# Kernel tuning notes

Measured on AMD Instinct MI355X. Metric: run time of the kernel, lower is better.

Reference implementation:

```python
import jax, jax.numpy as jnp
import numpy as np

N_NODES = 50000
N_EDGES = 625000
IN_DIM = 512
HID = 128
OUT_DIM = 40
N_LAYERS = 3


def setup_inputs() -> dict:
    key = jax.random.key(0)
    ks = jax.random.split(key, 12)
    features = jax.random.normal(ks[0], (N_NODES, IN_DIM), dtype=jnp.float32)
    src = jax.random.randint(ks[1], (N_EDGES,), 0, N_NODES, dtype=jnp.int32)
    dst = jax.random.randint(ks[2], (N_EDGES,), 0, N_NODES, dtype=jnp.int32)
    edge_w = jax.random.uniform(ks[3], (N_EDGES,), dtype=jnp.float32)
    s_in = 1.0 / np.sqrt(IN_DIM)
    s_h = 1.0 / np.sqrt(HID)
    emb_W = jax.random.uniform(ks[4], (IN_DIM, HID), jnp.float32, -s_in, s_in)
    emb_b = jax.random.uniform(ks[5], (HID,), jnp.float32, -s_in, s_in)
    W1 = jax.random.uniform(ks[6], (N_LAYERS, HID, HID), jnp.float32, -s_h, s_h)
    b1 = jax.random.uniform(ks[7], (N_LAYERS, HID), jnp.float32, -s_h, s_h)
    W2 = jax.random.uniform(ks[8], (N_LAYERS, HID, HID), jnp.float32, -s_h, s_h)
    b2 = jax.random.uniform(ks[9], (N_LAYERS, HID), jnp.float32, -s_h, s_h)
    ro_W = jax.random.uniform(ks[10], (HID, OUT_DIM), jnp.float32, -s_h, s_h)
    ro_b = jax.random.uniform(ks[11], (OUT_DIM,), jnp.float32, -s_h, s_h)
    return {"features": features, "src": src, "dst": dst, "edge_w": edge_w,
            "emb_W": emb_W, "emb_b": emb_b, "W1": W1, "b1": b1,
            "W2": W2, "b2": b2, "ro_W": ro_W, "ro_b": ro_b}


def reference(features, src, dst, edge_w, emb_W, emb_b, W1, b1, W2, b2, ro_W, ro_b):
    # Input embedding: [N, in_dim] -> [N, hid]
    h = features @ emb_W + emb_b
    n = h.shape[0]
    for l in range(N_LAYERS):
        # GINConv (sum aggregator, eps=0): agg_i = sum_{(u->i)} w * h_u
        msg = h[src] * edge_w[:, None]                      # [E, hid]
        agg = jax.ops.segment_sum(msg, dst, num_segments=n)  # [N, hid]
        z = h + agg                                          # (1+eps)*h + agg
        # apply_func MLP: Linear -> ReLU -> Linear, then outer ReLU
        z = jax.nn.relu(z @ W1[l] + b1[l]) @ W2[l] + b2[l]
        h = jax.nn.relu(z)
    return h @ ro_W + ro_b
```

## Files before the change

kernel.cpp:

```cpp
#include <hip/hip_runtime.h>

#define NN 50000
#define NE 625000
#define IND 512
#define HID 128
#define OUTD 40
#define NL 3
#define NB 196

typedef short v8s __attribute__((ext_vector_type(8)));
typedef float v4f __attribute__((ext_vector_type(4)));
typedef const __attribute__((address_space(1))) unsigned int gu32;
typedef __attribute__((address_space(3))) unsigned int lu32;

#define MFMA __builtin_amdgcn_mfma_f32_16x16x32_bf16

__device__ inline ushort f2bf(float x) {
    unsigned u = __float_as_uint(x);
    u += 0x7FFF + ((u >> 16) & 1);
    return (ushort)(u >> 16);
}
__device__ inline float bf2f(ushort b) { return __uint_as_float(((unsigned)b) << 16); }

__device__ inline void split8(float4 a, float4 b, v8s& hi, v8s& lo) {
    float v[8] = {a.x, a.y, a.z, a.w, b.x, b.y, b.z, b.w};
    v8s h, l;
#pragma unroll
    for (int i = 0; i < 8; i++) {
        ushort hu = f2bf(v[i]);
        h[i] = (short)hu;
        l[i] = (short)f2bf(v[i] - bf2f(hu));
    }
    hi = h;
    lo = l;
}

template <int NI, int NT>
__device__ inline void stage(const ushort* __restrict__ g, ushort* l, int tid) {
    const int wbase = tid & ~63;
#pragma unroll
    for (int j = 0; j < NI; j++) {
        __builtin_amdgcn_global_load_lds(
            (gu32*)((const char*)g + (size_t)(j * NT + tid) * 16),
            (lu32*)((char*)l + (j * NT + wbase) * 16), 16, 0, 0);
    }
}


__global__ __launch_bounds__(256) void count_kernel(const int* __restrict__ dst,
                                                    int* __restrict__ deg) {
    int e = blockIdx.x * 256 + threadIdx.x;
    if (e < NE) atomicAdd(&deg[dst[e]], 1);
}

__global__ __launch_bounds__(256) void scan1(const int* __restrict__ deg,
                                             int* __restrict__ ex,
                                             int* __restrict__ bsum) {
    __shared__ int s[256];
    int t = threadIdx.x;
    int idx = blockIdx.x * 256 + t;
    int d = idx < NN ? deg[idx] : 0;
    s[t] = d;
    __syncthreads();
#pragma unroll
    for (int off = 1; off < 256; off <<= 1) {
        int v = (t >= off) ? s[t - off] : 0;
        __syncthreads();
        s[t] += v;
        __syncthreads();
    }
    if (idx < NN) ex[idx] = s[t] - d;
    if (t == 255) bsum[blockIdx.x] = s[255];
}

__global__ __launch_bounds__(256) void scan2(const int* __restrict__ bsum,
                                             int* __restrict__ bpre) {
    __shared__ int s[256];
    int t = threadIdx.x;
    int d = t < NB ? bsum[t] : 0;
    s[t] = d;
    __syncthreads();
#pragma unroll
    for (int off = 1; off < 256; off <<= 1) {
        int v = (t >= off) ? s[t - off] : 0;
        __syncthreads();
        s[t] += v;
        __syncthreads();
    }
    if (t < NB) bpre[t] = s[t] - d;
}

__global__ __launch_bounds__(256) void scan3(const int* __restrict__ deg,
                                             const int* __restrict__ ex,
                                             const int* __restrict__ bpre,
                                             int* __restrict__ rp,
                                             int* __restrict__ cursor) {
    int idx = blockIdx.x * 256 + threadIdx.x;
    if (idx < NN) {
        int v = ex[idx] + bpre[blockIdx.x];
        rp[idx] = v;
        cursor[idx] = v;
        if (idx == NN - 1) rp[NN] = v + deg[idx];
    }
}

__global__ __launch_bounds__(256) void fill_kernel(const int* __restrict__ src,
                                                   const int* __restrict__ dst,
                                                   const float* __restrict__ ew,
                                                   int* __restrict__ cursor,
                                                   int2* __restrict__ csr) {
    int e = blockIdx.x * 256 + threadIdx.x;
    if (e < NE) {
        int d = dst[e];
        int pos = atomicAdd(&cursor[d], 1);
        csr[pos] = make_int2(src[e], __float_as_int(ew[e]));
    }
}


__global__ __launch_bounds__(256) void conv_emb(const float* __restrict__ W,
                                                ushort* __restrict__ P) {
    int idx = blockIdx.x * 256 + threadIdx.x;
    int k = idx >> 7;
    int c = idx & 127;
    float v = W[(size_t)k * HID + c];
    ushort hb = f2bf(v);
    ushort lb = f2bf(v - bf2f(hb));
    int it = k >> 6, kl = k & 63;
    int pos = it * 16384 + c * 64 + (kl ^ ((c & 7) << 3));
    P[pos] = hb;
    P[pos + 8192] = lb;
}

__global__ __launch_bounds__(256) void conv_mlp(const float* __restrict__ W1,
                                                const float* __restrict__ W2,
                                                ushort* __restrict__ P) {
    int idx = blockIdx.x * 256 + threadIdx.x;
    int lg = idx >> 14;
    int r = idx & 16383;
    int k = r >> 7, c = r & 127;
    int l = lg >> 1, g = lg & 1;
    const float* src = (g ? W2 : W1) + (size_t)l * HID * HID;
    float v = src[(size_t)k * HID + c];
    ushort hb = f2bf(v);
    ushort lb = f2bf(v - bf2f(hb));
    int q = c >> 5, cl = c & 31;
    int pos = lg * 32768 + q * 8192 + cl * 128 + (k ^ ((c & 7) << 3));
    P[pos] = hb;
    P[pos + 4096] = lb;
}

__global__ __launch_bounds__(256) void conv_ro(const float* __restrict__ W,
                                               ushort* __restrict__ Th,
                                               ushort* __restrict__ Tl) {
    int idx = blockIdx.x * 256 + threadIdx.x;
    int c = idx >> 7;
    int kk = idx & 127;
    float v = (c < OUTD) ? W[(size_t)kk * OUTD + c] : 0.f;
    ushort h = f2bf(v);
    Th[idx] = h;
    Tl[idx] = f2bf(v - bf2f(h));
}


__global__ __launch_bounds__(512) void emb_mfma(const float* __restrict__ X,
                                                const ushort* __restrict__ Wp,
                                                const float* __restrict__ B,
                                                float* __restrict__ H) {
    __shared__ __align__(16) ushort Wb[2][16384];
    const int tid = threadIdx.x;
    const int wid = tid >> 6, lane = tid & 63;
    const int lane15 = lane & 15, kg = (lane >> 4) * 8;
    const int swc = (lane15 & 7) << 3;
    const int brow = blockIdx.x * 128;
    const int grow = brow + wid * 16 + lane15;
    const float* xr = X + (size_t)(grow < NN ? grow : 0) * IND + kg;

    v4f acc[8];
#pragma unroll
    for (int i = 0; i < 8; i++) acc[i] = (v4f)0.f;

    float4 x0 = *reinterpret_cast<const float4*>(xr);
    float4 x1 = *reinterpret_cast<const float4*>(xr + 4);
    float4 x2 = *reinterpret_cast<const float4*>(xr + 32);
    float4 x3 = *reinterpret_cast<const float4*>(xr + 36);
    stage<4, 512>(Wp, &Wb[0][0], tid);

    for (int it = 0; it < 8; ++it) {
        float4 n0, n1, n2, n3;
        if (it < 7) {
            const float* xn = xr + (it + 1) * 64;
            n0 = *reinterpret_cast<const float4*>(xn);
            n1 = *reinterpret_cast<const float4*>(xn + 4);
            n2 = *reinterpret_cast<const float4*>(xn + 32);
            n3 = *reinterpret_cast<const float4*>(xn + 36);
            stage<4, 512>(Wp + (size_t)(it + 1) * 16384, &Wb[(it + 1) & 1][0], tid);
            asm volatile("s_waitcnt vmcnt(8)" ::: "memory");
        } else {
            asm volatile("s_waitcnt vmcnt(0)" ::: "memory");
        }
        __builtin_amdgcn_s_barrier();
        v8s ah0, al0, ah1, al1;
        split8(x0, x1, ah0, al0);
        split8(x2, x3, ah1, al1);
        const ushort* cb = &Wb[it & 1][0];
        const int s0 = kg ^ swc;
        const int s1 = (32 + kg) ^ swc;
        __builtin_amdgcn_s_setprio(1);
#pragma unroll
        for (int nf = 0; nf < 8; nf++) {
            int rb = (nf * 16 + lane15) * 64;
            v8s bh0 = *reinterpret_cast<const v8s*>(&cb[rb + s0]);
            v8s bl0 = *reinterpret_cast<const v8s*>(&cb[8192 + rb + s0]);
            v8s bh1 = *reinterpret_cast<const v8s*>(&cb[rb + s1]);
            v8s bl1 = *reinterpret_cast<const v8s*>(&cb[8192 + rb + s1]);
            v4f a = acc[nf];
            a = MFMA(ah0, bh0, a, 0, 0, 0);
            a = MFMA(al0, bh0, a, 0, 0, 0);
            a = MFMA(ah0, bl0, a, 0, 0, 0);
            a = MFMA(ah1, bh1, a, 0, 0, 0);
            a = MFMA(al1, bh1, a, 0, 0, 0);
            a = MFMA(ah1, bl1, a, 0, 0, 0);
            acc[nf] = a;
        }
        __builtin_amdgcn_s_setprio(0);
        asm volatile("s_waitcnt lgkmcnt(0)" ::: "memory");
        __builtin_amdgcn_s_barrier();
        x0 = n0; x1 = n1; x2 = n2; x3 = n3;
    }
#pragma unroll
    for (int nf = 0; nf < 8; nf++) {
        int col = nf * 16 + lane15;
        float bias = B[col];
#pragma unroll
        for (int r = 0; r < 4; r++) {
            int g = brow + wid * 16 + (lane >> 4) * 4 + r;
            if (g < NN) H[(size_t)g * HID + col] = acc[nf][r] + bias;
        }
    }
}


__global__ __launch_bounds__(256) void agg_kernel(const float* __restrict__ h,
                                                  const int* __restrict__ rp,
                                                  const int2* __restrict__ csr,
                                                  float* __restrict__ z) {
    const int node = blockIdx.x * 8 + (threadIdx.x >> 5);
    const int c4 = (threadIdx.x & 31) << 2;
    const float* hp = h + c4;
    v4f a0 = *reinterpret_cast<const v4f*>(hp + (size_t)node * HID);
    v4f a1 = (v4f)0.f, a2 = (v4f)0.f, a3 = (v4f)0.f;
    int k = rp[node];
    const int ke = rp[node + 1];
    for (; k + 7 < ke; k += 8) {
        int2 e0 = csr[k], e1 = csr[k + 1], e2 = csr[k + 2], e3 = csr[k + 3];
        int2 e4 = csr[k + 4], e5 = csr[k + 5], e6 = csr[k + 6], e7 = csr[k + 7];
        const v4f v0 = *reinterpret_cast<const v4f*>(hp + (size_t)e0.x * HID);
        const v4f v1 = *reinterpret_cast<const v4f*>(hp + (size_t)e1.x * HID);
        const v4f v2 = *reinterpret_cast<const v4f*>(hp + (size_t)e2.x * HID);
        const v4f v3 = *reinterpret_cast<const v4f*>(hp + (size_t)e3.x * HID);
        const v4f v4 = *reinterpret_cast<const v4f*>(hp + (size_t)e4.x * HID);
        const v4f v5 = *reinterpret_cast<const v4f*>(hp + (size_t)e5.x * HID);
        const v4f v6 = *reinterpret_cast<const v4f*>(hp + (size_t)e6.x * HID);
        const v4f v7 = *reinterpret_cast<const v4f*>(hp + (size_t)e7.x * HID);
        a0 += __int_as_float(e0.y) * v0;
        a1 += __int_as_float(e1.y) * v1;
        a2 += __int_as_float(e2.y) * v2;
        a3 += __int_as_float(e3.y) * v3;
        a0 += __int_as_float(e4.y) * v4;
        a1 += __int_as_float(e5.y) * v5;
        a2 += __int_as_float(e6.y) * v6;
        a3 += __int_as_float(e7.y) * v7;
    }
    for (; k + 1 < ke; k += 2) {
        int2 e0 = csr[k], e1 = csr[k + 1];
        a0 += __int_as_float(e0.y) * *reinterpret_cast<const v4f*>(hp + (size_t)e0.x * HID);
        a1 += __int_as_float(e1.y) * *reinterpret_cast<const v4f*>(hp + (size_t)e1.x * HID);
    }
    if (k < ke) {
        int2 e = csr[k];
        a0 += __int_as_float(e.y) * *reinterpret_cast<const v4f*>(hp + (size_t)e.x * HID);
    }
    *reinterpret_cast<v4f*>(z + (size_t)node * HID + c4) = (a0 + a1) + (a2 + a3);
}


template <int LAST>
__global__ __launch_bounds__(256) void mlp_mfma(const float* __restrict__ Z,
                                                const ushort* __restrict__ Wlp,
                                                const float* __restrict__ B1,
                                                const float* __restrict__ B2,
                                                const ushort* __restrict__ RWh,
                                                const ushort* __restrict__ RWl,
                                                const float* __restrict__ RB,
                                                float* __restrict__ H,
                                                float* __restrict__ OUT) {
    __shared__ __align__(16) ushort Wb[3][8192];
    __shared__ __align__(16) ushort Hh[64 * 128];
    __shared__ __align__(16) ushort Hl[64 * 128];
    const int tid = threadIdx.x;
    const int wid = tid >> 6, lane = tid & 63;
    const int lane15 = lane & 15, kg = (lane >> 4) * 8;
    const int swc = (lane15 & 7) << 3;
    const int brow = blockIdx.x * 64;
    const int grow = brow + wid * 16 + lane15;
    const int rowl = wid * 16 + lane15;
    const int sw = (rowl & 7) << 3;

    const float* zr = Z + (size_t)(grow < NN ? grow : 0) * HID + kg;
    float4 za[4], zb[4];
#pragma unroll
    for (int ks = 0; ks < 4; ks++) {
        za[ks] = *reinterpret_cast<const float4*>(zr + ks * 32);
        zb[ks] = *reinterpret_cast<const float4*>(zr + ks * 32 + 4);
    }
    stage<4, 256>(Wlp, &Wb[0][0], tid);
    stage<4, 256>(Wlp + 8192, &Wb[1][0], tid);

    v8s ah[4], al[4];
    v4f acc[8];
#pragma unroll
    for (int i = 0; i < 8; i++) acc[i] = (v4f)0.f;

#pragma unroll
    for (int q = 0; q < 8; q++) {
        if (q < 6) {
            stage<4, 256>(Wlp + (size_t)(q + 2) * 8192, &Wb[(q + 2) % 3][0], tid);
            asm volatile("s_waitcnt vmcnt(8)" ::: "memory");
        } else if (q == 6) {
            asm volatile("s_waitcnt vmcnt(4)" ::: "memory");
        } else {
            asm volatile("s_waitcnt vmcnt(0)" ::: "memory");
        }
        __builtin_amdgcn_s_barrier();
        if (q == 0) {
#pragma unroll
            for (int ks = 0; ks < 4; ks++) split8(za[ks], zb[ks], ah[ks], al[ks]);
        }
        if (q == 4) {
#pragma unroll
            for (int ks = 0; ks < 4; ks++) {
                int idx = rowl * 128 + ((ks * 32 + kg) ^ sw);
                ah[ks] = *reinterpret_cast<const v8s*>(&Hh[idx]);
                al[ks] = *reinterpret_cast<const v8s*>(&Hl[idx]);
            }
        }
        const ushort* cb = &Wb[q % 3][0];
        const int nfb = (q & 3) * 2;
        __builtin_amdgcn_s_setprio(1);
#pragma unroll
        for (int t = 0; t < 2; t++) {
            int rb = (t * 16 + lane15) * 128;
            v4f a = acc[nfb + t];
#pragma unroll
            for (int ks = 0; ks < 4; ks++) {
                int s = (ks * 32 + kg) ^ swc;
                v8s bh = *reinterpret_cast<const v8s*>(&cb[rb + s]);
                v8s bl = *reinterpret_cast<const v8s*>(&cb[4096 + rb + s]);
                a = MFMA(ah[ks], bh, a, 0, 0, 0);
                a = MFMA(al[ks], bh, a, 0, 0, 0);
                a = MFMA(ah[ks], bl, a, 0, 0, 0);
            }
            acc[nfb + t] = a;
        }
        __builtin_amdgcn_s_setprio(0);
        if (q < 4) {
#pragma unroll
            for (int t = 0; t < 2; t++) {
                int nf = nfb + t;
                int col = nf * 16 + lane15;
                float b = B1[col];
#pragma unroll
                for (int r = 0; r < 4; r++) {
                    int rl2 = wid * 16 + (lane >> 4) * 4 + r;
                    float v = acc[nf][r] + b;
                    v = v > 0.f ? v : 0.f;
                    ushort hb = f2bf(v);
                    int idx = rl2 * 128 + (col ^ ((rl2 & 7) << 3));
                    Hh[idx] = hb;
                    Hl[idx] = f2bf(v - bf2f(hb));
                }
                acc[nf] = (v4f)0.f;
            }
        } else if (LAST == 0) {
#pragma unroll
            for (int t = 0; t < 2; t++) {
                int nf = nfb + t;
                int col = nf * 16 + lane15;
                float b = B2[col];
#pragma unroll
                for (int r = 0; r < 4; r++) {
                    int g = brow + wid * 16 + (lane >> 4) * 4 + r;
                    if (g < NN) H[(size_t)g * HID + col] = fmaxf(acc[nf][r] + b, 0.f);
                }
            }
        } else {
#pragma unroll
            for (int t = 0; t < 2; t++) {
                int nf = nfb + t;
                int col = nf * 16 + lane15;
                float b = B2[col];
#pragma unroll
                for (int r = 0; r < 4; r++) {
                    int rl2 = wid * 16 + (lane >> 4) * 4 + r;
                    float v = fmaxf(acc[nf][r] + b, 0.f);
                    ushort hb = f2bf(v);
                    int idx = rl2 * 128 + (col ^ ((rl2 & 7) << 3));
                    Hh[idx] = hb;
                    Hl[idx] = f2bf(v - bf2f(hb));
                }
            }
        }
        asm volatile("s_waitcnt lgkmcnt(0)" ::: "memory");
        __builtin_amdgcn_s_barrier();
    }

    if (LAST) {
#pragma unroll
        for (int ks = 0; ks < 4; ks++) {
            int idx = rowl * 128 + ((ks * 32 + kg) ^ sw);
            ah[ks] = *reinterpret_cast<const v8s*>(&Hh[idx]);
            al[ks] = *reinterpret_cast<const v8s*>(&Hl[idx]);
        }
        v4f a3[3];
#pragma unroll
        for (int i = 0; i < 3; i++) a3[i] = (v4f)0.f;
#pragma unroll
        for (int nf = 0; nf < 3; nf++) {
            const ushort* bp = RWh + (size_t)(nf * 16 + lane15) * HID + kg;
            const ushort* bq = RWl + (size_t)(nf * 16 + lane15) * HID + kg;
            v4f a = a3[nf];
#pragma unroll
            for (int ks = 0; ks < 4; ks++) {
                v8s bh = *reinterpret_cast<const v8s*>(bp + ks * 32);
                v8s bl = *reinterpret_cast<const v8s*>(bq + ks * 32);
                a = MFMA(ah[ks], bh, a, 0, 0, 0);
                a = MFMA(al[ks], bh, a, 0, 0, 0);
                a = MFMA(ah[ks], bl, a, 0, 0, 0);
            }
            a3[nf] = a;
        }
#pragma unroll
        for (int nf = 0; nf < 3; nf++) {
            int col = nf * 16 + lane15;
            if (col < OUTD) {
                float b = RB[col];
#pragma unroll
                for (int r = 0; r < 4; r++) {
                    int g = brow + wid * 16 + (lane >> 4) * 4 + r;
                    if (g < NN) OUT[(size_t)g * OUTD + col] = a3[nf][r] + b;
                }
            }
        }
    }
}


extern "C" void kernel_launch(void* const* d_in, const int* in_sizes, int n_in,
                              void* d_out, int out_size, void* d_ws, size_t ws_size,
                              hipStream_t stream) {
    const float* features = (const float*)d_in[0];
    const int* src = (const int*)d_in[1];
    const int* dst = (const int*)d_in[2];
    const float* ew = (const float*)d_in[3];
    const float* embW = (const float*)d_in[4];
    const float* embB = (const float*)d_in[5];
    const float* W1 = (const float*)d_in[6];
    const float* B1 = (const float*)d_in[7];
    const float* W2 = (const float*)d_in[8];
    const float* B2 = (const float*)d_in[9];
    const float* roW = (const float*)d_in[10];
    const float* roB = (const float*)d_in[11];
    float* out = (float*)d_out;

    float* h = (float*)d_ws;
    float* z = h + (size_t)NN * HID;
    int* rp = (int*)(z + (size_t)NN * HID);
    int2* csr = (int2*)(rp + NN + 16);
    int* cursor = (int*)(csr + NE);
    int* deg = cursor + NN;
    int* ex = deg + NN;
    int* bsum = ex + NN;
    int* bpre = bsum + NB + 4;
    ushort* Wemb_p = (ushort*)(bpre + NB + 4);
    ushort* Wmlp_p = Wemb_p + 8 * 16384;
    ushort* roWt_h = Wmlp_p + (size_t)NL * 8 * 8192;
    ushort* roWt_l = roWt_h + 48 * 128;

    conv_emb<<<256, 256, 0, stream>>>(embW, Wemb_p);
    conv_mlp<<<384, 256, 0, stream>>>(W1, W2, Wmlp_p);
    conv_ro<<<24, 256, 0, stream>>>(roW, roWt_h, roWt_l);

    hipMemsetAsync(deg, 0, NN * sizeof(int), stream);
    count_kernel<<<(NE + 255) / 256, 256, 0, stream>>>(dst, deg);
    scan1<<<NB, 256, 0, stream>>>(deg, ex, bsum);
    scan2<<<1, 256, 0, stream>>>(bsum, bpre);
    scan3<<<NB, 256, 0, stream>>>(deg, ex, bpre, rp, cursor);
    fill_kernel<<<(NE + 255) / 256, 256, 0, stream>>>(src, dst, ew, cursor, csr);

    emb_mfma<<<(NN + 127) / 128, 512, 0, stream>>>(features, Wemb_p, embB, h);

    for (int l = 0; l < NL; l++) {
        agg_kernel<<<NN / 8, 256, 0, stream>>>(h, rp, csr, z);
        const ushort* wl = Wmlp_p + (size_t)l * 8 * 8192;
        const float* b1 = B1 + (size_t)l * HID;
        const float* b2 = B2 + (size_t)l * HID;
        if (l < NL - 1) {
            mlp_mfma<0><<<(NN + 63) / 64, 256, 0, stream>>>(
                z, wl, b1, b2, roWt_h, roWt_l, roB, h, out);
        } else {
            mlp_mfma<1><<<(NN + 63) / 64, 256, 0, stream>>>(
                z, wl, b1, b2, roWt_h, roWt_l, roB, h, out);
        }
    }
}
```

Baseline: 512.4 us.

## Fuse neighbor aggregation into the MLP kernel with ping-pong hidden buffers

Moves the per-node weighted neighbor gather-sum into the start of the MLP MFMA kernel. Each block aggregates its 64 rows directly into the swizzled bf16 hi/lo shared-memory tiles, so the separate agg kernel and its fp32 z round trip through global memory go away. Two hidden-state buffers alternate between layers so a layer never reads rows that another block is overwriting. In exchange, each block now has only 256 threads doing the latency-bound gather for 64 nodes, which lowers gather parallelism and may serialize the gather ahead of the GEMM.

After: 539.0 us. 1.05x slower.

```diff
diff --git a/kernel.cpp b/kernel.cpp
--- a/kernel.cpp
+++ b/kernel.cpp
@@ -241,59 +241,17 @@
 }
 
 
-__global__ __launch_bounds__(256) void agg_kernel(const float* __restrict__ h,
-                                                  const int* __restrict__ rp,
-                                                  const int2* __restrict__ csr,
-                                                  float* __restrict__ z) {
-    const int node = blockIdx.x * 8 + (threadIdx.x >> 5);
-    const int c4 = (threadIdx.x & 31) << 2;
-    const float* hp = h + c4;
-    v4f a0 = *reinterpret_cast<const v4f*>(hp + (size_t)node * HID);
-    v4f a1 = (v4f)0.f, a2 = (v4f)0.f, a3 = (v4f)0.f;
-    int k = rp[node];
-    const int ke = rp[node + 1];
-    for (; k + 7 < ke; k += 8) {
-        int2 e0 = csr[k], e1 = csr[k + 1], e2 = csr[k + 2], e3 = csr[k + 3];
-        int2 e4 = csr[k + 4], e5 = csr[k + 5], e6 = csr[k + 6], e7 = csr[k + 7];
-        const v4f v0 = *reinterpret_cast<const v4f*>(hp + (size_t)e0.x * HID);
-        const v4f v1 = *reinterpret_cast<const v4f*>(hp + (size_t)e1.x * HID);
-        const v4f v2 = *reinterpret_cast<const v4f*>(hp + (size_t)e2.x * HID);
-        const v4f v3 = *reinterpret_cast<const v4f*>(hp + (size_t)e3.x * HID);
-        const v4f v4 = *reinterpret_cast<const v4f*>(hp + (size_t)e4.x * HID);
-        const v4f v5 = *reinterpret_cast<const v4f*>(hp + (size_t)e5.x * HID);
-        const v4f v6 = *reinterpret_cast<const v4f*>(hp + (size_t)e6.x * HID);
-        const v4f v7 = *reinterpret_cast<const v4f*>(hp + (size_t)e7.x * HID);
-        a0 += __int_as_float(e0.y) * v0;
-        a1 += __int_as_float(e1.y) * v1;
-        a2 += __int_as_float(e2.y) * v2;
-        a3 += __int_as_float(e3.y) * v3;
-        a0 += __int_as_float(e4.y) * v4;
-        a1 += __int_as_float(e5.y) * v5;
-        a2 += __int_as_float(e6.y) * v6;
-        a3 += __int_as_float(e7.y) * v7;
-    }
-    for (; k + 1 < ke; k += 2) {
-        int2 e0 = csr[k], e1 = csr[k + 1];
-        a0 += __int_as_float(e0.y) * *reinterpret_cast<const v4f*>(hp + (size_t)e0.x * HID);
-        a1 += __int_as_float(e1.y) * *reinterpret_cast<const v4f*>(hp + (size_t)e1.x * HID);
-    }
-    if (k < ke) {
-        int2 e = csr[k];
-        a0 += __int_as_float(e.y) * *reinterpret_cast<const v4f*>(hp + (size_t)e.x * HID);
-    }
-    *reinterpret_cast<v4f*>(z + (size_t)node * HID + c4) = (a0 + a1) + (a2 + a3);
-}
-
-
 template <int LAST>
-__global__ __launch_bounds__(256) void mlp_mfma(const float* __restrict__ Z,
+__global__ __launch_bounds__(256) void mlp_mfma(const float* __restrict__ Hin,
+                                                const int* __restrict__ rp,
+                                                const int2* __restrict__ csr,
                                                 const ushort* __restrict__ Wlp,
                                                 const float* __restrict__ B1,
                                                 const float* __restrict__ B2,
                                                 const ushort* __restrict__ RWh,
                                                 const ushort* __restrict__ RWl,
                                                 const float* __restrict__ RB,
-                                                float* __restrict__ H,
+                                                float* __restrict__ Hout,
                                                 float* __restrict__ OUT) {
     __shared__ __align__(16) ushort Wb[3][8192];
     __shared__ __align__(16) ushort Hh[64 * 128];
@@ -303,21 +261,76 @@
     const int lane15 = lane & 15, kg = (lane >> 4) * 8;
     const int swc = (lane15 & 7) << 3;
     const int brow = blockIdx.x * 64;
-    const int grow = brow + wid * 16 + lane15;
     const int rowl = wid * 16 + lane15;
     const int sw = (rowl & 7) << 3;
 
-    const float* zr = Z + (size_t)(grow < NN ? grow : 0) * HID + kg;
-    float4 za[4], zb[4];
-#pragma unroll
-    for (int ks = 0; ks < 4; ks++) {
-        za[ks] = *reinterpret_cast<const float4*>(zr + ks * 32);
-        zb[ks] = *reinterpret_cast<const float4*>(zr + ks * 32 + 4);
-    }
     stage<4, 256>(Wlp, &Wb[0][0], tid);
     stage<4, 256>(Wlp + 8192, &Wb[1][0], tid);
 
+    const int hw = tid >> 5;
+    const int c4 = (tid & 31) << 2;
+    const float* hp = Hin + c4;
+#pragma unroll
+    for (int i = 0; i < 8; i++) {
+        const int nl = hw * 8 + i;
+        const int g = brow + nl;
+        v4f a0 = (v4f)0.f, a1 = (v4f)0.f, a2 = (v4f)0.f, a3 = (v4f)0.f;
+        if (g < NN) {
+            a0 = *reinterpret_cast<const v4f*>(hp + (size_t)g * HID);
+            int k = rp[g];
+            const int ke = rp[g + 1];
+            for (; k + 7 < ke; k += 8) {
+                int2 e0 = csr[k], e1 = csr[k + 1], e2 = csr[k + 2], e3 = csr[k + 3];
+                int2 e4 = csr[k + 4], e5 = csr[k + 5], e6 = csr[k + 6], e7 = csr[k + 7];
+                const v4f v0 = *reinterpret_cast<const v4f*>(hp + (size_t)e0.x * HID);
+                const v4f v1 = *reinterpret_cast<const v4f*>(hp + (size_t)e1.x * HID);
+                const v4f v2 = *reinterpret_cast<const v4f*>(hp + (size_t)e2.x * HID);
+                const v4f v3 = *reinterpret_cast<const v4f*>(hp + (size_t)e3.x * HID);
+                const v4f v4 = *reinterpret_cast<const v4f*>(hp + (size_t)e4.x * HID);
+                const v4f v5 = *reinterpret_cast<const v4f*>(hp + (size_t)e5.x * HID);
+                const v4f v6 = *reinterpret_cast<const v4f*>(hp + (size_t)e6.x * HID);
+                const v4f v7 = *reinterpret_cast<const v4f*>(hp + (size_t)e7.x * HID);
+                a0 += __int_as_float(e0.y) * v0;
+                a1 += __int_as_float(e1.y) * v1;
+                a2 += __int_as_float(e2.y) * v2;
+                a3 += __int_as_float(e3.y) * v3;
+                a0 += __int_as_float(e4.y) * v4;
+                a1 += __int_as_float(e5.y) * v5;
+                a2 += __int_as_float(e6.y) * v6;
+                a3 += __int_as_float(e7.y) * v7;
+            }
+            for (; k + 1 < ke; k += 2) {
+                int2 e0 = csr[k], e1 = csr[k + 1];
+                a0 += __int_as_float(e0.y) * *reinterpret_cast<const v4f*>(hp + (size_t)e0.x * HID);
+                a1 += __int_as_float(e1.y) * *reinterpret_cast<const v4f*>(hp + (size_t)e1.x * HID);
+            }
+            if (k < ke) {
+                int2 e = csr[k];
+                a0 += __int_as_float(e.y) * *reinterpret_cast<const v4f*>(hp + (size_t)e.x * HID);
+            }
+        }
+        v4f zv = (a0 + a1) + (a2 + a3);
+        ushort4 hh, ll;
+        {
+            ushort h0 = f2bf(zv[0]), h1 = f2bf(zv[1]), h2 = f2bf(zv[2]), h3 = f2bf(zv[3]);
+            hh = make_ushort4(h0, h1, h2, h3);
+            ll = make_ushort4(f2bf(zv[0] - bf2f(h0)), f2bf(zv[1] - bf2f(h1)),
+                              f2bf(zv[2] - bf2f(h2)), f2bf(zv[3] - bf2f(h3)));
+        }
+        const int idx = nl * 128 + (c4 ^ ((nl & 7) << 3));
+        *reinterpret_cast<ushort4*>(&Hh[idx]) = hh;
+        *reinterpret_cast<ushort4*>(&Hl[idx]) = ll;
+    }
+    __syncthreads();
+
     v8s ah[4], al[4];
+#pragma unroll
+    for (int ks = 0; ks < 4; ks++) {
+        int idx = rowl * 128 + ((ks * 32 + kg) ^ sw);
+        ah[ks] = *reinterpret_cast<const v8s*>(&Hh[idx]);
+        al[ks] = *reinterpret_cast<const v8s*>(&Hl[idx]);
+    }
+
     v4f acc[8];
 #pragma unroll
     for (int i = 0; i < 8; i++) acc[i] = (v4f)0.f;
@@ -333,10 +346,6 @@
             asm volatile("s_waitcnt vmcnt(0)" ::: "memory");
         }
         __builtin_amdgcn_s_barrier();
-        if (q == 0) {
-#pragma unroll
-            for (int ks = 0; ks < 4; ks++) split8(za[ks], zb[ks], ah[ks], al[ks]);
-        }
         if (q == 4) {
 #pragma unroll
             for (int ks = 0; ks < 4; ks++) {
@@ -391,7 +400,7 @@
 #pragma unroll
                 for (int r = 0; r < 4; r++) {
                     int g = brow + wid * 16 + (lane >> 4) * 4 + r;
-                    if (g < NN) H[(size_t)g * HID + col] = fmaxf(acc[nf][r] + b, 0.f);
+                    if (g < NN) Hout[(size_t)g * HID + col] = fmaxf(acc[nf][r] + b, 0.f);
                 }
             }
         } else {
@@ -473,9 +482,9 @@
     const float* roB = (const float*)d_in[11];
     float* out = (float*)d_out;
 
-    float* h = (float*)d_ws;
-    float* z = h + (size_t)NN * HID;
-    int* rp = (int*)(z + (size_t)NN * HID);
+    float* hA = (float*)d_ws;
+    float* hB = hA + (size_t)NN * HID;
+    int* rp = (int*)(hB + (size_t)NN * HID);
     int2* csr = (int2*)(rp + NN + 16);
     int* cursor = (int*)(csr + NE);
     int* deg = cursor + NN;
@@ -498,19 +507,15 @@
     scan3<<<NB, 256, 0, stream>>>(deg, ex, bpre, rp, cursor);
     fill_kernel<<<(NE + 255) / 256, 256, 0, stream>>>(src, dst, ew, cursor, csr);
 
-    emb_mfma<<<(NN + 127) / 128, 512, 0, stream>>>(features, Wemb_p, embB, h);
-
-    for (int l = 0; l < NL; l++) {
-        agg_kernel<<<NN / 8, 256, 0, stream>>>(h, rp, csr, z);
-        const ushort* wl = Wmlp_p + (size_t)l * 8 * 8192;
-        const float* b1 = B1 + (size_t)l * HID;
-        const float* b2 = B2 + (size_t)l * HID;
-        if (l < NL - 1) {
-            mlp_mfma<0><<<(NN + 63) / 64, 256, 0, stream>>>(
-                z, wl, b1, b2, roWt_h, roWt_l, roB, h, out);
-        } else {
-            mlp_mfma<1><<<(NN + 63) / 64, 256, 0, stream>>>(
-                z, wl, b1, b2, roWt_h, roWt_l, roB, h, out);
-        }
-    }
-}
+    emb_mfma<<<(NN + 127) / 128, 512, 0, stream>>>(features, Wemb_p, embB, hA);
+
+    const int grid = (NN + 63) / 64;
+    mlp_mfma<0><<<grid, 256, 0, stream>>>(hA, rp, csr, Wmlp_p, B1, B2,
+                                          roWt_h, roWt_l, roB, hB, out);
+    mlp_mfma<0><<<grid, 256, 0, stream>>>(hB, rp, csr, Wmlp_p + (size_t)8 * 8192,
+                                          B1 + HID, B2 + HID,
+                                          roWt_h, roWt_l, roB, hA, out);
+    mlp_mfma<1><<<grid, 256, 0, stream>>>(hA, rp, csr, Wmlp_p + (size_t)16 * 8192,
+                                          B1 + 2 * HID, B2 + 2 * HID,
+                                          roWt_h, roWt_l, roB, hB, out);
+}
```
